# Optimization experiments

Measured on AMD Instinct MI355X. Metric: run time of the kernel, lower is better.

Reference implementation:

```python
import jax, jax.numpy as jnp
import numpy as np
from math import factorial

D = 2          # qudit dimension
L = 13         # number of qudits: state dim = D**L = 8192
J, K = 0, 1    # levels coupled by the gate
CUTOFF = 10    # Taylor truncation order
INDEX = set(range(13))


def _series(z, parity):
    # sum_{i=1..CUTOFF, i%2==parity} z**i / i!   (truncated exp split into even/odd parts)
    s = jnp.zeros((), dtype=jnp.complex64)
    for i in range(1, CUTOFF + 1):
        if i % 2 == parity:
            s = s + z ** i / factorial(i)
    return s


def _gate(theta):
    # single-qudit RX gate matrix, truncated-Taylor version matching the torch code
    z = (-0.5j) * theta.astype(jnp.complex64)
    odd = _series(z, 1)   # ~ -i sin(theta/2)
    even = _series(z, 0)  # ~ cos(theta/2) - 1
    M = jnp.eye(D, dtype=jnp.complex64)
    M = M.at[J, K].add(odd)
    M = M.at[K, J].add(odd)
    M = M.at[J, J].add(even)
    M = M.at[K, K].add(even)
    return M


def setup_inputs() -> dict:
    key = jax.random.key(0)
    k1, k2, k3 = jax.random.split(key, 3)
    dim = D ** L
    return {
        "x_real": jax.random.normal(k1, (dim, 64), dtype=jnp.float32),
        "x_imag": jax.random.normal(k2, (dim, 64), dtype=jnp.float32),
        "angle": jax.random.normal(k3, (L,), dtype=jnp.float32),
    }


def reference(x_real, x_imag, angle):
    x = x_real.astype(jnp.complex64) + 1j * x_imag.astype(jnp.complex64)
    eye = jnp.eye(D, dtype=jnp.complex64)
    U = jnp.eye(1, dtype=jnp.complex64)
    for i in range(L):  # fixed structural loop over qudits (13 iterations)
        M = _gate(angle[i]) if i in INDEX else eye
        U = jnp.kron(U, M)
    out = U @ x  # [D^L, B] complex64
    return jnp.stack([out.real, out.imag])  # [2, D^L, B] float32
```

## Files before the change

### kernel.cpp

```cpp
#include <hip/hip_runtime.h>

#define PLANE (8192 * 64)

typedef float f4 __attribute__((ext_vector_type(4)));

__device__ __forceinline__ void gate_coeffs(float theta, float& a, float& s) {
    float t = 0.5f * theta;
    float u = t * t;
    s = t * (1.f + u * (-1.f/6.f + u * (1.f/120.f + u * (-1.f/5040.f + u * (1.f/362880.f)))));
    a = 1.f + u * (-0.5f + u * (1.f/24.f + u * (-1.f/720.f + u * (1.f/40320.f + u * (-1.f/3628800.f)))));
}

__device__ __forceinline__ void bf(f4& v0, f4& v1, float a, float s) {
    f4 n0, n1;
    n0.x = a * v0.x + s * v1.y;  n0.y = a * v0.y - s * v1.x;
    n0.z = a * v0.z + s * v1.w;  n0.w = a * v0.w - s * v1.z;
    n1.x = a * v1.x + s * v0.y;  n1.y = a * v1.y - s * v0.x;
    n1.z = a * v1.z + s * v0.w;  n1.w = a * v1.w - s * v0.z;
    v0 = n0; v1 = n1;
}

__global__ __launch_bounds__(256) void rx_low(const float* __restrict__ xr,
                                              const float* __restrict__ xi,
                                              const float* __restrict__ angle,
                                              f4* __restrict__ ws4) {
    __shared__ f4 l4[64 * 16];
    const int t = threadIdx.x, bid = blockIdx.x;
    const int g = bid >> 1, half = bid & 1;
    const int cp = t & 15, rq = t >> 4;

    const float2* xr2 = (const float2*)xr;
    const float2* xi2 = (const float2*)xi;

    {
        float a0, s0, a1, s1;
        gate_coeffs(angle[12], a0, s0);
        gate_coeffs(angle[11], a1, s1);
        f4 v[4];
        #pragma unroll
        for (int k = 0; k < 4; ++k) {
            int gi = (g * 64 + 4 * rq + k) * 32 + half * 16 + cp;
            float2 re = xr2[gi], im = xi2[gi];
            v[k] = (f4){re.x, im.x, re.y, im.y};
        }
        bf(v[0], v[1], a0, s0); bf(v[2], v[3], a0, s0);
        bf(v[0], v[2], a1, s1); bf(v[1], v[3], a1, s1);
        #pragma unroll
        for (int k = 0; k < 4; ++k) l4[(4 * rq + k) * 16 + cp] = v[k];
    }
    __syncthreads();

    {
        float a2, s2, a3, s3;
        gate_coeffs(angle[10], a2, s2);
        gate_coeffs(angle[9],  a3, s3);
        int base = ((rq >> 2) << 4) | (rq & 3);
        f4 w0 = l4[(base     ) * 16 + cp], w1 = l4[(base +  4) * 16 + cp];
        f4 w2 = l4[(base +  8) * 16 + cp], w3 = l4[(base + 12) * 16 + cp];
        bf(w0, w1, a2, s2); bf(w2, w3, a2, s2);
        bf(w0, w2, a3, s3); bf(w1, w3, a3, s3);
        l4[(base     ) * 16 + cp] = w0; l4[(base +  4) * 16 + cp] = w1;
        l4[(base +  8) * 16 + cp] = w2; l4[(base + 12) * 16 + cp] = w3;
    }
    __syncthreads();

    {
        float a4, s4, a5, s5;
        gate_coeffs(angle[8], a4, s4);
        gate_coeffs(angle[7], a5, s5);
        f4 w0 = l4[(rq     ) * 16 + cp], w1 = l4[(rq + 16) * 16 + cp];
        f4 w2 = l4[(rq + 32) * 16 + cp], w3 = l4[(rq + 48) * 16 + cp];
        bf(w0, w1, a4, s4); bf(w2, w3, a4, s4);
        bf(w0, w2, a5, s5); bf(w1, w3, a5, s5);
        const int cp32 = half * 16 + cp, q = cp32 >> 3, cb = cp32 & 7;
        const int e = g * 8 + cb;
        ws4[(size_t)((rq     ) * 4 + q) * 1024 + e] = w0;
        ws4[(size_t)((rq + 16) * 4 + q) * 1024 + e] = w1;
        ws4[(size_t)((rq + 32) * 4 + q) * 1024 + e] = w2;
        ws4[(size_t)((rq + 48) * 4 + q) * 1024 + e] = w3;
    }
}

__global__ __launch_bounds__(256) void rx_high(const float* __restrict__ angle,
                                               const f4* __restrict__ ws4,
                                               float* __restrict__ out) {
    __shared__ f4 l4[128 * 8];
    const int t = threadIdx.x, bid = blockIdx.x;
    const int m = bid >> 2, q = bid & 3;
    const int cp = t & 7, hq = t >> 3;

    {
        float a5, s5, a6, s6;
        gate_coeffs(angle[1], a5, s5);
        gate_coeffs(angle[0], a6, s6);
        const f4* src = ws4 + (size_t)(m * 4 + q) * 1024;
        f4 v0 = src[(hq     ) * 8 + cp], v1 = src[(hq + 32) * 8 + cp];
        f4 v2 = src[(hq + 64) * 8 + cp], v3 = src[(hq + 96) * 8 + cp];
        bf(v0, v1, a5, s5); bf(v2, v3, a5, s5);
        bf(v0, v2, a6, s6); bf(v1, v3, a6, s6);
        l4[(hq     ) * 8 + cp] = v0; l4[(hq + 32) * 8 + cp] = v1;
        l4[(hq + 64) * 8 + cp] = v2; l4[(hq + 96) * 8 + cp] = v3;
    }
    __syncthreads();

    {
        float a3, s3, a4, s4;
        gate_coeffs(angle[3], a3, s3);
        gate_coeffs(angle[2], a4, s4);
        int base = ((hq >> 3) << 5) | (hq & 7);
        f4 w0 = l4[(base     ) * 8 + cp], w1 = l4[(base +  8) * 8 + cp];
        f4 w2 = l4[(base + 16) * 8 + cp], w3 = l4[(base + 24) * 8 + cp];
        bf(w0, w1, a3, s3); bf(w2, w3, a3, s3);
        bf(w0, w2, a4, s4); bf(w1, w3, a4, s4);
        l4[(base     ) * 8 + cp] = w0; l4[(base +  8) * 8 + cp] = w1;
        l4[(base + 16) * 8 + cp] = w2; l4[(base + 24) * 8 + cp] = w3;
    }
    __syncthreads();

    {
        float a1, s1, a2, s2;
        gate_coeffs(angle[5], a1, s1);
        gate_coeffs(angle[4], a2, s2);
        int b = ((hq >> 1) << 3) | (hq & 1);
        f4 w0 = l4[(b    ) * 8 + cp], w1 = l4[(b + 2) * 8 + cp];
        f4 w2 = l4[(b + 4) * 8 + cp], w3 = l4[(b + 6) * 8 + cp];
        bf(w0, w1, a1, s1); bf(w2, w3, a1, s1);
        bf(w0, w2, a2, s2); bf(w1, w3, a2, s2);
        l4[(b    ) * 8 + cp] = w0; l4[(b + 2) * 8 + cp] = w1;
        l4[(b + 4) * 8 + cp] = w2; l4[(b + 6) * 8 + cp] = w3;
    }
    __syncthreads();

    {
        float a0, s0;
        gate_coeffs(angle[6], a0, s0);
        float2* outre2 = (float2*)out;
        float2* outim2 = (float2*)(out + PLANE);
        #pragma unroll
        for (int pp = 0; pp < 2; ++pp) {
            int hp = hq + 32 * pp;
            f4 w0 = l4[(2 * hp) * 8 + cp], w1 = l4[(2 * hp + 1) * 8 + cp];
            bf(w0, w1, a0, s0);
            int o = ((2 * hp) * 64 + m) * 32 + q * 8 + cp;
            outre2[o] = make_float2(w0.x, w0.z);
            outim2[o] = make_float2(w0.y, w0.w);
            outre2[o + 2048] = make_float2(w1.x, w1.z);
            outim2[o + 2048] = make_float2(w1.y, w1.w);
        }
    }
}

extern "C" void kernel_launch(void* const* d_in, const int* in_sizes, int n_in,
                              void* d_out, int out_size, void* d_ws, size_t ws_size,
                              hipStream_t stream) {
    const float* xr    = (const float*)d_in[0];
    const float* xi    = (const float*)d_in[1];
    const float* angle = (const float*)d_in[2];
    float* out = (float*)d_out;
    f4*    ws4 = (f4*)d_ws;

    rx_low <<<256, 256, 0, stream>>>(xr, xi, angle, ws4);
    rx_high<<<256, 256, 0, stream>>>(angle, ws4, out);
}
```

Before: 13.85 us.

## Fuse low and high gate kernels with a grid-wide atomic barrier

Merges the two kernels into one persistent launch of 256 blocks. Blocks exchange intermediates through the workspace using cache-bypassing (sc0 sc1) global stores and loads, and synchronize with a spin barrier over 8 padded atomic counters. The goal is to remove the second kernel launch and its inter-kernel gap. In exchange it adds a memset launch, the spin-wait cost, and a deadlock risk if not all 256 blocks are co-resident.

```diff
diff --git a/kernel.cpp b/kernel.cpp
--- a/kernel.cpp
+++ b/kernel.cpp
@@ -1,6 +1,7 @@
 #include <hip/hip_runtime.h>
 
 #define PLANE (8192 * 64)
+#define NBLK 256
 
 typedef float f4 __attribute__((ext_vector_type(4)));
 
@@ -20,19 +21,21 @@
     v0 = n0; v1 = n1;
 }
 
-__global__ __launch_bounds__(256) void rx_low(const float* __restrict__ xr,
-                                              const float* __restrict__ xi,
-                                              const float* __restrict__ angle,
-                                              f4* __restrict__ ws4) {
-    __shared__ f4 l4[64 * 16];
+__global__ __launch_bounds__(256) void rx_fused(const float* __restrict__ xr,
+                                                const float* __restrict__ xi,
+                                                const float* __restrict__ angle,
+                                                f4* __restrict__ ws4,
+                                                unsigned int* __restrict__ cnt,
+                                                float* __restrict__ out) {
+    __shared__ f4 l4[1024];
     const int t = threadIdx.x, bid = blockIdx.x;
-    const int g = bid >> 1, half = bid & 1;
-    const int cp = t & 15, rq = t >> 4;
-
-    const float2* xr2 = (const float2*)xr;
-    const float2* xi2 = (const float2*)xi;
 
     {
+        const int g = bid >> 1, half = bid & 1;
+        const int cp = t & 15, rq = t >> 4;
+        const float2* xr2 = (const float2*)xr;
+        const float2* xi2 = (const float2*)xi;
+
         float a0, s0, a1, s1;
         gate_coeffs(angle[12], a0, s0);
         gate_coeffs(angle[11], a1, s1);
@@ -47,105 +50,134 @@
         bf(v[0], v[2], a1, s1); bf(v[1], v[3], a1, s1);
         #pragma unroll
         for (int k = 0; k < 4; ++k) l4[(4 * rq + k) * 16 + cp] = v[k];
+        __syncthreads();
+
+        {
+            float a2, s2, a3, s3;
+            gate_coeffs(angle[10], a2, s2);
+            gate_coeffs(angle[9],  a3, s3);
+            int base = ((rq >> 2) << 4) | (rq & 3);
+            f4 w0 = l4[(base     ) * 16 + cp], w1 = l4[(base +  4) * 16 + cp];
+            f4 w2 = l4[(base +  8) * 16 + cp], w3 = l4[(base + 12) * 16 + cp];
+            bf(w0, w1, a2, s2); bf(w2, w3, a2, s2);
+            bf(w0, w2, a3, s3); bf(w1, w3, a3, s3);
+            l4[(base     ) * 16 + cp] = w0; l4[(base +  4) * 16 + cp] = w1;
+            l4[(base +  8) * 16 + cp] = w2; l4[(base + 12) * 16 + cp] = w3;
+        }
+        __syncthreads();
+
+        {
+            float a4, s4, a5, s5;
+            gate_coeffs(angle[8], a4, s4);
+            gate_coeffs(angle[7], a5, s5);
+            f4 w0 = l4[(rq     ) * 16 + cp], w1 = l4[(rq + 16) * 16 + cp];
+            f4 w2 = l4[(rq + 32) * 16 + cp], w3 = l4[(rq + 48) * 16 + cp];
+            bf(w0, w1, a4, s4); bf(w2, w3, a4, s4);
+            bf(w0, w2, a5, s5); bf(w1, w3, a5, s5);
+            const int cp32 = half * 16 + cp, q = cp32 >> 3, cb = cp32 & 7;
+            const int e = g * 8 + cb;
+            const f4* p0 = ws4 + ((size_t)((rq     ) * 4 + q) * 1024 + e);
+            const f4* p1 = ws4 + ((size_t)((rq + 16) * 4 + q) * 1024 + e);
+            const f4* p2 = ws4 + ((size_t)((rq + 32) * 4 + q) * 1024 + e);
+            const f4* p3 = ws4 + ((size_t)((rq + 48) * 4 + q) * 1024 + e);
+            asm volatile("global_store_dwordx4 %0, %4, off sc0 sc1\n\t"
+                         "global_store_dwordx4 %1, %5, off sc0 sc1\n\t"
+                         "global_store_dwordx4 %2, %6, off sc0 sc1\n\t"
+                         "global_store_dwordx4 %3, %7, off sc0 sc1"
+                         :: "v"(p0), "v"(p1), "v"(p2), "v"(p3),
+                            "v"(w0), "v"(w1), "v"(w2), "v"(w3) : "memory");
+        }
+    }
+
+    asm volatile("s_waitcnt vmcnt(0)" ::: "memory");
+    __syncthreads();
+    if (t == 0) {
+        __hip_atomic_fetch_add(cnt + (bid & 7) * 16, 1u,
+                               __ATOMIC_RELAXED, __HIP_MEMORY_SCOPE_AGENT);
+        unsigned int sum;
+        do {
+            __builtin_amdgcn_s_sleep(8);
+            sum = 0;
+            #pragma unroll
+            for (int i = 0; i < 8; ++i)
+                sum += __hip_atomic_load(cnt + i * 16,
+                                         __ATOMIC_RELAXED, __HIP_MEMORY_SCOPE_AGENT);
+        } while (sum < NBLK);
     }
     __syncthreads();
 
     {
-        float a2, s2, a3, s3;
-        gate_coeffs(angle[10], a2, s2);
-        gate_coeffs(angle[9],  a3, s3);
-        int base = ((rq >> 2) << 4) | (rq & 3);
-        f4 w0 = l4[(base     ) * 16 + cp], w1 = l4[(base +  4) * 16 + cp];
-        f4 w2 = l4[(base +  8) * 16 + cp], w3 = l4[(base + 12) * 16 + cp];
-        bf(w0, w1, a2, s2); bf(w2, w3, a2, s2);
-        bf(w0, w2, a3, s3); bf(w1, w3, a3, s3);
-        l4[(base     ) * 16 + cp] = w0; l4[(base +  4) * 16 + cp] = w1;
-        l4[(base +  8) * 16 + cp] = w2; l4[(base + 12) * 16 + cp] = w3;
-    }
-    __syncthreads();
+        const int m = bid >> 2, q = bid & 3;
+        const int cp = t & 7, hq = t >> 3;
 
-    {
-        float a4, s4, a5, s5;
-        gate_coeffs(angle[8], a4, s4);
-        gate_coeffs(angle[7], a5, s5);
-        f4 w0 = l4[(rq     ) * 16 + cp], w1 = l4[(rq + 16) * 16 + cp];
-        f4 w2 = l4[(rq + 32) * 16 + cp], w3 = l4[(rq + 48) * 16 + cp];
-        bf(w0, w1, a4, s4); bf(w2, w3, a4, s4);
-        bf(w0, w2, a5, s5); bf(w1, w3, a5, s5);
-        const int cp32 = half * 16 + cp, q = cp32 >> 3, cb = cp32 & 7;
-        const int e = g * 8 + cb;
-        ws4[(size_t)((rq     ) * 4 + q) * 1024 + e] = w0;
-        ws4[(size_t)((rq + 16) * 4 + q) * 1024 + e] = w1;
-        ws4[(size_t)((rq + 32) * 4 + q) * 1024 + e] = w2;
-        ws4[(size_t)((rq + 48) * 4 + q) * 1024 + e] = w3;
-    }
-}
+        {
+            float a5, s5, a6, s6;
+            gate_coeffs(angle[1], a5, s5);
+            gate_coeffs(angle[0], a6, s6);
+            const f4* src = ws4 + (size_t)(m * 4 + q) * 1024;
+            const f4* q0 = src + ((hq     ) * 8 + cp);
+            const f4* q1 = src + ((hq + 32) * 8 + cp);
+            const f4* q2 = src + ((hq + 64) * 8 + cp);
+            const f4* q3 = src + ((hq + 96) * 8 + cp);
+            f4 v0, v1, v2, v3;
+            asm volatile("global_load_dwordx4 %0, %4, off sc0 sc1\n\t"
+                         "global_load_dwordx4 %1, %5, off sc0 sc1\n\t"
+                         "global_load_dwordx4 %2, %6, off sc0 sc1\n\t"
+                         "global_load_dwordx4 %3, %7, off sc0 sc1\n\t"
+                         "s_waitcnt vmcnt(0)"
+                         : "=&v"(v0), "=&v"(v1), "=&v"(v2), "=&v"(v3)
+                         : "v"(q0), "v"(q1), "v"(q2), "v"(q3) : "memory");
+            bf(v0, v1, a5, s5); bf(v2, v3, a5, s5);
+            bf(v0, v2, a6, s6); bf(v1, v3, a6, s6);
+            l4[(hq     ) * 8 + cp] = v0; l4[(hq + 32) * 8 + cp] = v1;
+            l4[(hq + 64) * 8 + cp] = v2; l4[(hq + 96) * 8 + cp] = v3;
+        }
+        __syncthreads();
 
-__global__ __launch_bounds__(256) void rx_high(const float* __restrict__ angle,
-                                               const f4* __restrict__ ws4,
-                                               float* __restrict__ out) {
-    __shared__ f4 l4[128 * 8];
-    const int t = threadIdx.x, bid = blockIdx.x;
-    const int m = bid >> 2, q = bid & 3;
-    const int cp = t & 7, hq = t >> 3;
+        {
+            float a3, s3, a4, s4;
+            gate_coeffs(angle[3], a3, s3);
+            gate_coeffs(angle[2], a4, s4);
+            int base = ((hq >> 3) << 5) | (hq & 7);
+            f4 w0 = l4[(base     ) * 8 + cp], w1 = l4[(base +  8) * 8 + cp];
+            f4 w2 = l4[(base + 16) * 8 + cp], w3 = l4[(base + 24) * 8 + cp];
+            bf(w0, w1, a3, s3); bf(w2, w3, a3, s3);
+            bf(w0, w2, a4, s4); bf(w1, w3, a4, s4);
+            l4[(base     ) * 8 + cp] = w0; l4[(base +  8) * 8 + cp] = w1;
+            l4[(base + 16) * 8 + cp] = w2; l4[(base + 24) * 8 + cp] = w3;
+        }
+        __syncthreads();
 
-    {
-        float a5, s5, a6, s6;
-        gate_coeffs(angle[1], a5, s5);
-        gate_coeffs(angle[0], a6, s6);
-        const f4* src = ws4 + (size_t)(m * 4 + q) * 1024;
-        f4 v0 = src[(hq     ) * 8 + cp], v1 = src[(hq + 32) * 8 + cp];
-        f4 v2 = src[(hq + 64) * 8 + cp], v3 = src[(hq + 96) * 8 + cp];
-        bf(v0, v1, a5, s5); bf(v2, v3, a5, s5);
-        bf(v0, v2, a6, s6); bf(v1, v3, a6, s6);
-        l4[(hq     ) * 8 + cp] = v0; l4[(hq + 32) * 8 + cp] = v1;
-        l4[(hq + 64) * 8 + cp] = v2; l4[(hq + 96) * 8 + cp] = v3;
-    }
-    __syncthreads();
+        {
+            float a1, s1, a2, s2;
+            gate_coeffs(angle[5], a1, s1);
+            gate_coeffs(angle[4], a2, s2);
+            int b = ((hq >> 1) << 3) | (hq & 1);
+            f4 w0 = l4[(b    ) * 8 + cp], w1 = l4[(b + 2) * 8 + cp];
+            f4 w2 = l4[(b + 4) * 8 + cp], w3 = l4[(b + 6) * 8 + cp];
+            bf(w0, w1, a1, s1); bf(w2, w3, a1, s1);
+            bf(w0, w2, a2, s2); bf(w1, w3, a2, s2);
+            l4[(b    ) * 8 + cp] = w0; l4[(b + 2) * 8 + cp] = w1;
+            l4[(b + 4) * 8 + cp] = w2; l4[(b + 6) * 8 + cp] = w3;
+        }
+        __syncthreads();
 
-    {
-        float a3, s3, a4, s4;
-        gate_coeffs(angle[3], a3, s3);
-        gate_coeffs(angle[2], a4, s4);
-        int base = ((hq >> 3) << 5) | (hq & 7);
-        f4 w0 = l4[(base     ) * 8 + cp], w1 = l4[(base +  8) * 8 + cp];
-        f4 w2 = l4[(base + 16) * 8 + cp], w3 = l4[(base + 24) * 8 + cp];
-        bf(w0, w1, a3, s3); bf(w2, w3, a3, s3);
-        bf(w0, w2, a4, s4); bf(w1, w3, a4, s4);
-        l4[(base     ) * 8 + cp] = w0; l4[(base +  8) * 8 + cp] = w1;
-        l4[(base + 16) * 8 + cp] = w2; l4[(base + 24) * 8 + cp] = w3;
-    }
-    __syncthreads();
-
-    {
-        float a1, s1, a2, s2;
-        gate_coeffs(angle[5], a1, s1);
-        gate_coeffs(angle[4], a2, s2);
-        int b = ((hq >> 1) << 3) | (hq & 1);
-        f4 w0 = l4[(b    ) * 8 + cp], w1 = l4[(b + 2) * 8 + cp];
-        f4 w2 = l4[(b + 4) * 8 + cp], w3 = l4[(b + 6) * 8 + cp];
-        bf(w0, w1, a1, s1); bf(w2, w3, a1, s1);
-        bf(w0, w2, a2, s2); bf(w1, w3, a2, s2);
-        l4[(b    ) * 8 + cp] = w0; l4[(b + 2) * 8 + cp] = w1;
-        l4[(b + 4) * 8 + cp] = w2; l4[(b + 6) * 8 + cp] = w3;
-    }
-    __syncthreads();
-
-    {
-        float a0, s0;
-        gate_coeffs(angle[6], a0, s0);
-        float2* outre2 = (float2*)out;
-        float2* outim2 = (float2*)(out + PLANE);
-        #pragma unroll
-        for (int pp = 0; pp < 2; ++pp) {
-            int hp = hq + 32 * pp;
-            f4 w0 = l4[(2 * hp) * 8 + cp], w1 = l4[(2 * hp + 1) * 8 + cp];
-            bf(w0, w1, a0, s0);
-            int o = ((2 * hp) * 64 + m) * 32 + q * 8 + cp;
-            outre2[o] = make_float2(w0.x, w0.z);
-            outim2[o] = make_float2(w0.y, w0.w);
-            outre2[o + 2048] = make_float2(w1.x, w1.z);
-            outim2[o + 2048] = make_float2(w1.y, w1.w);
+        {
+            float a0, s0;
+            gate_coeffs(angle[6], a0, s0);
+            float2* outre2 = (float2*)out;
+            float2* outim2 = (float2*)(out + PLANE);
+            #pragma unroll
+            for (int pp = 0; pp < 2; ++pp) {
+                int hp = hq + 32 * pp;
+                f4 w0 = l4[(2 * hp) * 8 + cp], w1 = l4[(2 * hp + 1) * 8 + cp];
+                bf(w0, w1, a0, s0);
+                int o = ((2 * hp) * 64 + m) * 32 + q * 8 + cp;
+                outre2[o] = make_float2(w0.x, w0.z);
+                outim2[o] = make_float2(w0.y, w0.w);
+                outre2[o + 2048] = make_float2(w1.x, w1.z);
+                outim2[o + 2048] = make_float2(w1.y, w1.w);
+            }
         }
     }
 }
@@ -158,7 +190,8 @@
     const float* angle = (const float*)d_in[2];
     float* out = (float*)d_out;
     f4*    ws4 = (f4*)d_ws;
+    unsigned int* cnt = (unsigned int*)((char*)d_ws + (4u << 20));
 
-    rx_low <<<256, 256, 0, stream>>>(xr, xi, angle, ws4);
-    rx_high<<<256, 256, 0, stream>>>(angle, ws4, out);
+    hipMemsetAsync(cnt, 0, 512, stream);
+    rx_fused<<<NBLK, 256, 0, stream>>>(xr, xi, angle, ws4, cnt, out);
 }
```

Result: slower. 20.11 us (+45.2%).
